# Kernel tuning notes

Measured on AMD Instinct MI355X. Metric: run time of the kernel, lower is better.

The kernel has to match this reference:

```python
import jax, jax.numpy as jnp
import numpy as np

NUM_QUERIES, NUM_KEYS = 32, 64
QUERY_DIM, KEY_DIM = 512, 512
NUM_HEADS, ATTN_DIM = 8, 64
EMBED_DIM = NUM_HEADS * ATTN_DIM  # 512
OUT_DIM = 512
TEMPERATURE = float(np.sqrt(ATTN_DIM))


def setup_inputs() -> dict:
    key = jax.random.key(0)
    ks = jax.random.split(key, 6)
    b = 1.0 / TEMPERATURE
    b_p = 1.0 / float(np.sqrt(OUT_DIM))
    q = jax.random.normal(ks[0], (NUM_QUERIES, 2048, QUERY_DIM), dtype=jnp.float32)
    k = jax.random.normal(ks[1], (NUM_KEYS, 2048, KEY_DIM), dtype=jnp.float32)
    query_weight = jax.random.uniform(ks[2], (NUM_QUERIES, QUERY_DIM, EMBED_DIM), minval=-b, maxval=b, dtype=jnp.float32)
    key_weight = jax.random.uniform(ks[3], (NUM_KEYS, KEY_DIM, EMBED_DIM), minval=-b, maxval=b, dtype=jnp.float32)
    value_weight = jax.random.uniform(ks[4], (NUM_KEYS, KEY_DIM, EMBED_DIM), minval=-b, maxval=b, dtype=jnp.float32)
    proj_weight = jax.random.uniform(ks[5], (NUM_QUERIES, EMBED_DIM, OUT_DIM), minval=-b_p, maxval=b_p, dtype=jnp.float32)
    return {"q": q, "k": k, "query_weight": query_weight, "key_weight": key_weight,
            "value_weight": value_weight, "proj_weight": proj_weight}


def reference(q, k, query_weight, key_weight, value_weight, proj_weight):
    Qn, bs, _ = q.shape
    Kn = k.shape[0]
    H, D = NUM_HEADS, ATTN_DIM
    # per-slot projections: (slots, bs, embed) -> split embed into heads
    query = jnp.einsum('ibq,iqe->ibe', q, query_weight).reshape(Qn, bs, H, D)
    key_e = jnp.einsum('jbk,jke->jbe', k, key_weight).reshape(Kn, bs, H, D)
    value = jnp.einsum('jbk,jke->jbe', k, value_weight).reshape(Kn, bs, H, D)
    # logits over key slots per (batch, head, query slot)
    logits = jnp.einsum('ibhd,jbhd->bhij', query, key_e) / TEMPERATURE
    attn = jax.nn.softmax(logits, axis=-1)  # softmax over key slots
    out = jnp.einsum('bhij,jbhd->ibhd', attn, value).reshape(Qn, bs, H * D)
    out = jnp.einsum('ibe,ieo->ibo', out, proj_weight)
    return out
```

## Files before the change

kernel.cpp:

```cpp
#include <hip/hip_runtime.h>

typedef __attribute__((ext_vector_type(8))) short bf16x8;
typedef __attribute__((ext_vector_type(4))) float f32x4;
typedef __attribute__((ext_vector_type(4))) unsigned short us4;

__device__ __forceinline__ unsigned short f2bf(float f) {
    unsigned u = __builtin_bit_cast(unsigned, f);
    u += 0x7FFFu + ((u >> 16) & 1u);
    return (unsigned short)(u >> 16);
}

__device__ __forceinline__ void gl_lds16(const void* g, void* l) {
    __builtin_amdgcn_global_load_lds(
        (const __attribute__((address_space(1))) unsigned int*)g,
        (__attribute__((address_space(3))) unsigned int*)l, 16, 0, 0);
}

#define FENCE_ asm volatile("" ::: "memory")
#define BAR_ do { FENCE_; __builtin_amdgcn_s_barrier(); FENCE_; } while (0)

__global__ __launch_bounds__(256) void cast_f32_bf16(const float* __restrict__ in,
                                                     unsigned short* __restrict__ out, int n4) {
    int i = blockIdx.x * blockDim.x + threadIdx.x;
    int stride = gridDim.x * blockDim.x;
    for (; i < n4; i += stride) {
        float4 v = ((const float4*)in)[i];
        us4 o;
        o.x = f2bf(v.x); o.y = f2bf(v.y); o.z = f2bf(v.z); o.w = f2bf(v.w);
        ((us4*)out)[i] = o;
    }
}

__global__ __launch_bounds__(256) void transpose_w(const float* __restrict__ wq,
                                                   const float* __restrict__ wk,
                                                   const float* __restrict__ wv,
                                                   const float* __restrict__ wp,
                                                   unsigned short* __restrict__ Wt) {
    int sb = blockIdx.x >> 6;
    int tile = blockIdx.x & 63;
    const float* src;
    if (sb < 32)       src = wq + (size_t)sb * 262144;
    else if (sb < 96)  src = wk + (size_t)(sb - 32) * 262144;
    else if (sb < 160) src = wv + (size_t)(sb - 96) * 262144;
    else               src = wp + (size_t)(sb - 160) * 262144;
    unsigned short* dst = Wt + (size_t)sb * 262144;
    int q0 = (tile & 7) * 64, e0 = (tile >> 3) * 64;
    __shared__ float t[64][65];
    int tx = threadIdx.x & 63, ty = threadIdx.x >> 6;
    for (int i = 0; i < 16; i++) {
        int r = ty + 4 * i;
        t[r][tx] = src[(size_t)(q0 + r) * 512 + e0 + tx];
    }
    __syncthreads();
    int tx2 = threadIdx.x & 31, ty2 = threadIdx.x >> 5;
    for (int i = 0; i < 8; i++) {
        int e = ty2 + 8 * i;
        int qq = tx2 * 2;
        unsigned a = f2bf(t[qq][e]);
        unsigned bb = f2bf(t[qq + 1][e]);
        *(unsigned*)&dst[(size_t)(e0 + e) * 512 + q0 + qq] = a | (bb << 16);
    }
}

__device__ __forceinline__ void gemm256(const unsigned short* __restrict__ Ag,
                                        const unsigned short* __restrict__ Bg,
                                        unsigned short (&lds)[2][2][16384],
                                        f32x4 (&acc)[8][4]) {
    const int tid = threadIdx.x;
    const int l = tid & 63, wid = tid >> 6;
    const int wr = (wid >> 2) * 128, wc = (wid & 3) * 64;
    const int lr = l & 15, shi = l >> 4;
    const int srcs = ((l & 7) ^ ((l >> 3) & 7)) * 8;
    const int grow = l >> 3;

    bf16x8 af[4][2], bf[4][2];

#define STG_(which, hh, t) do {                                                     \
    const unsigned short* gp = (which) ? Bg : Ag;                                   \
    _Pragma("unroll")                                                               \
    for (int q = 0; q < 2; q++) {                                                   \
        int lrow = (hh) * 128 + wid * 16 + q * 8;                                   \
        gl_lds16(gp + (size_t)(lrow + grow) * 512 + (t) * 64 + srcs,                \
                 &lds[(t) & 1][which][lrow * 64]);                                  \
    } } while (0)

#define LDA_(cur, mh) do {                                                          \
    _Pragma("unroll") for (int m = 0; m < 4; m++)                                   \
    _Pragma("unroll") for (int ks = 0; ks < 2; ks++)                                \
        af[m][ks] = *(const bf16x8*)&lds[cur][0]                                    \
            [(wr + (mh) * 64 + m * 16 + lr) * 64 + ((ks * 4 + shi) ^ (l & 7)) * 8]; \
    } while (0)

#define LDB_(cur) do {                                                             \
    _Pragma("unroll") for (int n = 0; n < 4; n++)                                   \
    _Pragma("unroll") for (int ks = 0; ks < 2; ks++)                                \
        bf[n][ks] = *(const bf16x8*)&lds[cur][1]                                    \
            [(wc + n * 16 + lr) * 64 + ((ks * 4 + shi) ^ (l & 7)) * 8];             \
    } while (0)

#define MM_(mh) do {                                                                \
    __builtin_amdgcn_s_setprio(1);                                                  \
    _Pragma("unroll") for (int m = 0; m < 4; m++)                                   \
    _Pragma("unroll") for (int n = 0; n < 4; n++)                                   \
    _Pragma("unroll") for (int ks = 0; ks < 2; ks++)                                \
        acc[(mh) * 4 + m][n] = __builtin_amdgcn_mfma_f32_16x16x32_bf16(             \
            af[m][ks], bf[n][ks], acc[(mh) * 4 + m][n], 0, 0, 0);                   \
    __builtin_amdgcn_s_setprio(0);                                                  \
    } while (0)

    STG_(0, 0, 0); STG_(0, 1, 0);
    STG_(1, 0, 0); STG_(1, 1, 0);
    STG_(1, 0, 1); STG_(1, 1, 1);
    asm volatile("s_waitcnt vmcnt(4)" ::: "memory");
    BAR_;

#pragma unroll
    for (int t = 0; t < 8; t++) {
        const int cur = t & 1;
        if (t < 7) { STG_(0, 0, t + 1); STG_(0, 1, t + 1); }
        LDA_(cur, 0); LDB_(cur);
        BAR_; MM_(0); BAR_;
        if (t < 6) { STG_(1, 0, t + 2); STG_(1, 1, t + 2); }
        LDA_(cur, 1);
        BAR_; MM_(1);
        if (t < 6)       asm volatile("s_waitcnt vmcnt(4)" ::: "memory");
        else if (t == 6) asm volatile("s_waitcnt vmcnt(0)" ::: "memory");
        if (t < 7) BAR_;
    }
#undef STG_
#undef LDA_
#undef LDB_
#undef MM_
}

__global__ __launch_bounds__(512, 1) void gemm_qkv(const unsigned short* __restrict__ qb,
                                                   const unsigned short* __restrict__ kb,
                                                   const unsigned short* __restrict__ Wt,
                                                   unsigned short* __restrict__ Qs,
                                                   unsigned short* __restrict__ Ks,
                                                   unsigned short* __restrict__ Vs) {
    __shared__ __align__(16) unsigned short lds[2][2][16384];
    int bid = blockIdx.x;
    int logical = (bid & 7) * 320 + (bid >> 3);
    int sIdx, x;
    if (logical < 512) {
        int grp = logical >> 5, w = logical & 31;
        sIdx = grp * 2 + (w & 1);
        x = w >> 1;
    } else {
        int p = (logical - 512) >> 5, w = (logical - 512) & 31;
        sIdx = 32 + p * 2 + (w & 1);
        x = w >> 1;
    }
    int tm = x >> 1, tn = x & 1;
    const unsigned short* A;
    unsigned short* Cw;
    int wslot;
    if (sIdx < 32) {
        A = qb + (size_t)sIdx * 1048576; Cw = Qs + (size_t)sIdx * 1048576; wslot = sIdx;
    } else {
        int pp = sIdx - 32, ks = pp >> 1;
        A = kb + (size_t)ks * 1048576;
        if (pp & 1) { Cw = Vs + (size_t)ks * 1048576; wslot = 96 + ks; }
        else        { Cw = Ks + (size_t)ks * 1048576; wslot = 32 + ks; }
    }
    const unsigned short* B = Wt + (size_t)wslot * 262144;
    const unsigned short* Ag = A + (size_t)(tm * 256) * 512;
    const unsigned short* Bg = B + (size_t)(tn * 256) * 512;

    f32x4 acc[8][4] = {};
    gemm256(Ag, Bg, lds, acc);

    const int l = threadIdx.x & 63, wid = threadIdx.x >> 6;
    const int wm = wid >> 2, wc = (wid & 3) * 64;
    unsigned short* Cs = &lds[0][0][0];
    for (int pass = 0; pass < 2; pass++) {
        __syncthreads();
        if (wm == pass) {
            for (int m = 0; m < 8; m++)
                for (int n = 0; n < 4; n++)
                    for (int r = 0; r < 4; r++)
                        Cs[(m * 16 + (l >> 4) * 4 + r) * 264 + wc + n * 16 + (l & 15)] = f2bf(acc[m][n][r]);
        }
        __syncthreads();
        for (int rnd = 0; rnd < 8; rnd++) {
            int idx = rnd * 512 + threadIdx.x;
            int row = idx >> 5, c8 = (idx & 31) * 8;
            bf16x8 v = *(const bf16x8*)&Cs[row * 264 + c8];
            *(bf16x8*)&Cw[(size_t)(tm * 256 + pass * 128 + row) * 512 + tn * 256 + c8] = v;
        }
    }
}

__global__ __launch_bounds__(512, 1) void gemm_proj(const unsigned short* __restrict__ Ain,
                                                    const unsigned short* __restrict__ Wt,
                                                    float* __restrict__ out) {
    __shared__ __align__(16) unsigned short lds[2][2][16384];
    int bid = blockIdx.x;
    int logical = (bid & 7) * 64 + (bid >> 3);
    int s = logical >> 4, x = logical & 15;
    int tm = x >> 1, tn = x & 1;
    const unsigned short* A = Ain + (size_t)s * 1048576;
    const unsigned short* B = Wt + (size_t)(160 + s) * 262144;
    const unsigned short* Ag = A + (size_t)(tm * 256) * 512;
    const unsigned short* Bg = B + (size_t)(tn * 256) * 512;

    f32x4 acc[8][4] = {};
    gemm256(Ag, Bg, lds, acc);

    const int l = threadIdx.x & 63, wid = threadIdx.x >> 6;
    const int wm = wid >> 2, wc = (wid & 3) * 64;
    float* Cf = (float*)&lds[0][0][0];
    for (int pass = 0; pass < 4; pass++) {
        __syncthreads();
        if (wm == (pass >> 1)) {
            int mb = (pass & 1) * 4;
            for (int mm = 0; mm < 4; mm++)
                for (int n = 0; n < 4; n++)
                    for (int r = 0; r < 4; r++)
                        Cf[(mm * 16 + (l >> 4) * 4 + r) * 260 + wc + n * 16 + (l & 15)] = acc[mb + mm][n][r];
        }
        __syncthreads();
        for (int rnd = 0; rnd < 8; rnd++) {
            int idx = rnd * 512 + threadIdx.x;
            int row = idx >> 6, c4 = (idx & 63) * 4;
            float4 v = *(const float4*)&Cf[row * 260 + c4];
            *(float4*)&out[(size_t)s * 1048576 + (size_t)(tm * 256 + pass * 64 + row) * 512 + tn * 256 + c4] = v;
        }
    }
}

__global__ __launch_bounds__(256) void attn_k(const unsigned short* __restrict__ Qs,
                                              const unsigned short* __restrict__ Ks,
                                              const unsigned short* __restrict__ Vs,
                                              unsigned short* __restrict__ Aout) {
    __shared__ __align__(16) unsigned short pl[4][32 * 72];
    __shared__ __align__(16) unsigned short vt[4][64 * 88];
    const size_t SL = 1048576;
    int w = threadIdx.x >> 6, l = threadIdx.x & 63;
    int g = blockIdx.x * 4 + w;
    int b = g >> 3, h = g & 7;
    const unsigned short* Qp = Qs + (size_t)b * 512 + h * 64;
    const unsigned short* Kp = Ks + (size_t)b * 512 + h * 64;
    const unsigned short* Vp = Vs + (size_t)b * 512 + h * 64;
    int lr = l & 15, lc = l >> 4;
    unsigned short* vtw = vt[w];

    for (int jr = 0; jr < 64; jr += 8) {
        int j = jr + (l >> 3), d0 = (l & 7) * 8;
        bf16x8 v = *(const bf16x8*)&Vp[(size_t)j * SL + d0];
        for (int e = 0; e < 8; e++) vtw[(d0 + e) * 88 + j] = (unsigned short)v[e];
    }

    bf16x8 aQ[2][2], bK[4][2];
    for (int m = 0; m < 2; m++)
        for (int kc = 0; kc < 2; kc++)
            aQ[m][kc] = *(const bf16x8*)&Qp[(size_t)(m * 16 + lr) * SL + kc * 32 + lc * 8];
    for (int n = 0; n < 4; n++)
        for (int kc = 0; kc < 2; kc++)
            bK[n][kc] = *(const bf16x8*)&Kp[(size_t)(n * 16 + lr) * SL + kc * 32 + lc * 8];

    f32x4 acc[2][4] = {};
    for (int kc = 0; kc < 2; kc++)
        for (int m = 0; m < 2; m++)
            for (int n = 0; n < 4; n++)
                acc[m][n] = __builtin_amdgcn_mfma_f32_16x16x32_bf16(aQ[m][kc], bK[n][kc], acc[m][n], 0, 0, 0);

    const float sc = 0.18033688011112042f;
    for (int m = 0; m < 2; m++) {
        for (int r = 0; r < 4; r++) {
            float v = acc[m][0][r];
            for (int n = 1; n < 4; n++) v = fmaxf(v, acc[m][n][r]);
            for (int sh = 1; sh < 16; sh <<= 1) v = fmaxf(v, __shfl_xor(v, sh));
            float ssum = 0.f;
            for (int n = 0; n < 4; n++) {
                float p = exp2f((acc[m][n][r] - v) * sc);
                acc[m][n][r] = p;
                ssum += p;
            }
            for (int sh = 1; sh < 16; sh <<= 1) ssum += __shfl_xor(ssum, sh);
            float inv = 1.0f / ssum;
            for (int n = 0; n < 4; n++)
                pl[w][(m * 16 + lc * 4 + r) * 72 + n * 16 + lr] = f2bf(acc[m][n][r] * inv);
        }
    }

    bf16x8 aP[2][2], bV[4][2];
    for (int m = 0; m < 2; m++)
        for (int kc = 0; kc < 2; kc++)
            aP[m][kc] = *(const bf16x8*)&pl[w][(m * 16 + lr) * 72 + kc * 32 + lc * 8];
    for (int n = 0; n < 4; n++)
        for (int kc = 0; kc < 2; kc++)
            bV[n][kc] = *(const bf16x8*)&vtw[(n * 16 + lr) * 88 + kc * 32 + lc * 8];

    f32x4 o[2][4] = {};
    for (int kc = 0; kc < 2; kc++)
        for (int m = 0; m < 2; m++)
            for (int n = 0; n < 4; n++)
                o[m][n] = __builtin_amdgcn_mfma_f32_16x16x32_bf16(aP[m][kc], bV[n][kc], o[m][n], 0, 0, 0);

    for (int m = 0; m < 2; m++)
        for (int n = 0; n < 4; n++)
            for (int r = 0; r < 4; r++)
                vtw[(m * 16 + lc * 4 + r) * 88 + n * 16 + lr] = f2bf(o[m][n][r]);
    for (int rnd = 0; rnd < 4; rnd++) {
        int i = rnd * 8 + (l >> 3), d0 = (l & 7) * 8;
        bf16x8 v = *(const bf16x8*)&vtw[i * 88 + d0];
        *(bf16x8*)&Aout[(size_t)i * SL + (size_t)b * 512 + h * 64 + d0] = v;
    }
}

extern "C" void kernel_launch(void* const* d_in, const int* in_sizes, int n_in,
                              void* d_out, int out_size, void* d_ws, size_t ws_size,
                              hipStream_t stream) {
    const float* q  = (const float*)d_in[0];
    const float* k  = (const float*)d_in[1];
    const float* wq = (const float*)d_in[2];
    const float* wk = (const float*)d_in[3];
    const float* wv = (const float*)d_in[4];
    const float* wp = (const float*)d_in[5];

    char* ws = (char*)d_ws;
    unsigned short* qb = (unsigned short*)(ws);
    unsigned short* kb = (unsigned short*)(ws + ((size_t)64 << 20));
    unsigned short* Wt = (unsigned short*)(ws + ((size_t)192 << 20));
    unsigned short* Qs = (unsigned short*)(ws + ((size_t)288 << 20));
    unsigned short* Ks = (unsigned short*)(ws + ((size_t)352 << 20));
    unsigned short* Vs = (unsigned short*)(ws + ((size_t)480 << 20));
    unsigned short* Aout = qb;
    float* out = (float*)d_out;

    hipLaunchKernelGGL(cast_f32_bf16, dim3(2048), dim3(256), 0, stream, q, qb, 32 * 2048 * 512 / 4);
    hipLaunchKernelGGL(cast_f32_bf16, dim3(2048), dim3(256), 0, stream, k, kb, 64 * 2048 * 512 / 4);
    hipLaunchKernelGGL(transpose_w, dim3(192 * 64), dim3(256), 0, stream, wq, wk, wv, wp, Wt);
    hipLaunchKernelGGL(gemm_qkv, dim3(2560), dim3(512), 0, stream, qb, kb, Wt, Qs, Ks, Vs);
    hipLaunchKernelGGL(attn_k, dim3(4096), dim3(256), 0, stream, Qs, Ks, Vs, Aout);
    hipLaunchKernelGGL(gemm_proj, dim3(512), dim3(512), 0, stream, Aout, Wt, out);
}
```

Before: 554.4 us.

## Fuse f32-to-bf16 input casting into QKV GEMM A-tile loading

Removes the two standalone cast kernels and instead has the QKV GEMM load fp32 activations into registers, convert them with packed bf16 conversion instructions, and write them into swizzled LDS, while B tiles still use direct global-to-LDS loads. This drops a full read/write pass over the 384 MB of q/k data plus the intermediate bf16 buffers. In exchange, A traffic doubles in bytes per GEMM tile, since each A tile is reread by the two N-tiles as fp32. The change also uses more registers for staging and needs extra VALU conversion work inside the pipelined loop.

```diff
diff --git a/kernel.cpp b/kernel.cpp
--- a/kernel.cpp
+++ b/kernel.cpp
@@ -18,18 +18,6 @@
 
 #define FENCE_ asm volatile("" ::: "memory")
 #define BAR_ do { FENCE_; __builtin_amdgcn_s_barrier(); FENCE_; } while (0)
-
-__global__ __launch_bounds__(256) void cast_f32_bf16(const float* __restrict__ in,
-                                                     unsigned short* __restrict__ out, int n4) {
-    int i = blockIdx.x * blockDim.x + threadIdx.x;
-    int stride = gridDim.x * blockDim.x;
-    for (; i < n4; i += stride) {
-        float4 v = ((const float4*)in)[i];
-        us4 o;
-        o.x = f2bf(v.x); o.y = f2bf(v.y); o.z = f2bf(v.z); o.w = f2bf(v.w);
-        ((us4*)out)[i] = o;
-    }
-}
 
 __global__ __launch_bounds__(256) void transpose_w(const float* __restrict__ wq,
                                                    const float* __restrict__ wk,
@@ -133,8 +121,111 @@
 #undef MM_
 }
 
-__global__ __launch_bounds__(512, 1) void gemm_qkv(const unsigned short* __restrict__ qb,
-                                                   const unsigned short* __restrict__ kb,
+__device__ __forceinline__ void gemm256f(const float* __restrict__ Af,
+                                         const unsigned short* __restrict__ Bg,
+                                         unsigned short (&lds)[2][2][16384],
+                                         f32x4 (&acc)[8][4]) {
+    const int tid = threadIdx.x;
+    const int l = tid & 63, wid = tid >> 6;
+    const int wr = (wid >> 2) * 128, wc = (wid & 3) * 64;
+    const int lr = l & 15, shi = l >> 4;
+    const int srcs = ((l & 7) ^ ((l >> 3) & 7)) * 8;
+    const int grow = l >> 3;
+    const int aswz = ((l & 7) ^ ((l >> 3) & 7)) * 8;
+
+    float4 rS0[8], rS1[8];
+    bf16x8 af[4][2], bf[4][2];
+
+#define LOADA_(S, t) do {                                                           \
+    _Pragma("unroll") for (int j = 0; j < 4; j++) {                                 \
+        const float* rp = Af + (size_t)(wid * 32 + j * 8 + (l >> 3)) * 512          \
+                          + (t) * 64 + (l & 7) * 8;                                 \
+        S[j * 2]     = *(const float4*)rp;                                          \
+        S[j * 2 + 1] = *(const float4*)(rp + 4);                                    \
+    } } while (0)
+
+#define WRITEA_(S, t) do {                                                          \
+    _Pragma("unroll") for (int j = 0; j < 4; j++) {                                 \
+        int row_ = wid * 32 + j * 8 + (l >> 3);                                     \
+        unsigned p0, p1, p2, p3;                                                    \
+        asm("v_cvt_pk_bf16_f32 %0, %1, %2" : "=v"(p0) : "v"(S[j*2].x),   "v"(S[j*2].y));   \
+        asm("v_cvt_pk_bf16_f32 %0, %1, %2" : "=v"(p1) : "v"(S[j*2].z),   "v"(S[j*2].w));   \
+        asm("v_cvt_pk_bf16_f32 %0, %1, %2" : "=v"(p2) : "v"(S[j*2+1].x), "v"(S[j*2+1].y)); \
+        asm("v_cvt_pk_bf16_f32 %0, %1, %2" : "=v"(p3) : "v"(S[j*2+1].z), "v"(S[j*2+1].w)); \
+        uint4 pk_; pk_.x = p0; pk_.y = p1; pk_.z = p2; pk_.w = p3;                  \
+        *(uint4*)&lds[(t) & 1][0][row_ * 64 + aswz] = pk_;                          \
+    } } while (0)
+
+#define STGB_(hh, t) do {                                                           \
+    _Pragma("unroll")                                                               \
+    for (int q = 0; q < 2; q++) {                                                   \
+        int lrow = (hh) * 128 + wid * 16 + q * 8;                                   \
+        gl_lds16(Bg + (size_t)(lrow + grow) * 512 + (t) * 64 + srcs,                \
+                 &lds[(t) & 1][1][lrow * 64]);                                      \
+    } } while (0)
+
+#define LDA_(cur, mh) do {                                                          \
+    _Pragma("unroll") for (int m = 0; m < 4; m++)                                   \
+    _Pragma("unroll") for (int ks = 0; ks < 2; ks++)                                \
+        af[m][ks] = *(const bf16x8*)&lds[cur][0]                                    \
+            [(wr + (mh) * 64 + m * 16 + lr) * 64 + ((ks * 4 + shi) ^ (l & 7)) * 8]; \
+    } while (0)
+
+#define LDB_(cur) do {                                                             \
+    _Pragma("unroll") for (int n = 0; n < 4; n++)                                   \
+    _Pragma("unroll") for (int ks = 0; ks < 2; ks++)                                \
+        bf[n][ks] = *(const bf16x8*)&lds[cur][1]                                    \
+            [(wc + n * 16 + lr) * 64 + ((ks * 4 + shi) ^ (l & 7)) * 8];             \
+    } while (0)
+
+#define MM_(mh) do {                                                                \
+    __builtin_amdgcn_s_setprio(1);                                                  \
+    _Pragma("unroll") for (int m = 0; m < 4; m++)                                   \
+    _Pragma("unroll") for (int n = 0; n < 4; n++)                                   \
+    _Pragma("unroll") for (int ks = 0; ks < 2; ks++)                                \
+        acc[(mh) * 4 + m][n] = __builtin_amdgcn_mfma_f32_16x16x32_bf16(             \
+            af[m][ks], bf[n][ks], acc[(mh) * 4 + m][n], 0, 0, 0);                   \
+    __builtin_amdgcn_s_setprio(0);                                                  \
+    } while (0)
+
+    LOADA_(rS0, 0); STGB_(0, 0); STGB_(1, 0);
+    LOADA_(rS1, 1); STGB_(0, 1); STGB_(1, 1);
+    WRITEA_(rS0, 0);
+    asm volatile("s_waitcnt lgkmcnt(0)" ::: "memory");
+    asm volatile("s_waitcnt vmcnt(12)" ::: "memory");
+    BAR_;
+
+#pragma unroll
+    for (int t = 0; t < 8; t++) {
+        const int cur = t & 1;
+        if (t < 7) {
+            if (((t + 1) & 1) == 0) WRITEA_(rS0, t + 1);
+            else                    WRITEA_(rS1, t + 1);
+        }
+        LDA_(cur, 0); LDB_(cur);
+        BAR_; MM_(0); BAR_;
+        if (t < 6) {
+            if (((t + 2) & 1) == 0) LOADA_(rS0, t + 2);
+            else                    LOADA_(rS1, t + 2);
+            STGB_(0, t + 2); STGB_(1, t + 2);
+        }
+        LDA_(cur, 1);
+        BAR_; MM_(1);
+        asm volatile("s_waitcnt lgkmcnt(0)" ::: "memory");
+        if (t < 6)       asm volatile("s_waitcnt vmcnt(12)" ::: "memory");
+        else if (t == 6) asm volatile("s_waitcnt vmcnt(0)" ::: "memory");
+        if (t < 7) BAR_;
+    }
+#undef LOADA_
+#undef WRITEA_
+#undef STGB_
+#undef LDA_
+#undef LDB_
+#undef MM_
+}
+
+__global__ __launch_bounds__(512, 1) void gemm_qkv(const float* __restrict__ qf,
+                                                   const float* __restrict__ kf,
                                                    const unsigned short* __restrict__ Wt,
                                                    unsigned short* __restrict__ Qs,
                                                    unsigned short* __restrict__ Ks,
@@ -153,23 +244,23 @@
         x = w >> 1;
     }
     int tm = x >> 1, tn = x & 1;
-    const unsigned short* A;
+    const float* Afull;
     unsigned short* Cw;
     int wslot;
     if (sIdx < 32) {
-        A = qb + (size_t)sIdx * 1048576; Cw = Qs + (size_t)sIdx * 1048576; wslot = sIdx;
+        Afull = qf + (size_t)sIdx * 1048576; Cw = Qs + (size_t)sIdx * 1048576; wslot = sIdx;
     } else {
         int pp = sIdx - 32, ks = pp >> 1;
-        A = kb + (size_t)ks * 1048576;
+        Afull = kf + (size_t)ks * 1048576;
         if (pp & 1) { Cw = Vs + (size_t)ks * 1048576; wslot = 96 + ks; }
         else        { Cw = Ks + (size_t)ks * 1048576; wslot = 32 + ks; }
     }
     const unsigned short* B = Wt + (size_t)wslot * 262144;
-    const unsigned short* Ag = A + (size_t)(tm * 256) * 512;
+    const float* Ag = Afull + (size_t)(tm * 256) * 512;
     const unsigned short* Bg = B + (size_t)(tn * 256) * 512;
 
     f32x4 acc[8][4] = {};
-    gemm256(Ag, Bg, lds, acc);
+    gemm256f(Ag, Bg, lds, acc);
 
     const int l = threadIdx.x & 63, wid = threadIdx.x >> 6;
     const int wm = wid >> 2, wc = (wid & 3) * 64;
@@ -321,19 +412,15 @@
     const float* wp = (const float*)d_in[5];
 
     char* ws = (char*)d_ws;
-    unsigned short* qb = (unsigned short*)(ws);
-    unsigned short* kb = (unsigned short*)(ws + ((size_t)64 << 20));
+    unsigned short* Aout = (unsigned short*)(ws);
     unsigned short* Wt = (unsigned short*)(ws + ((size_t)192 << 20));
     unsigned short* Qs = (unsigned short*)(ws + ((size_t)288 << 20));
     unsigned short* Ks = (unsigned short*)(ws + ((size_t)352 << 20));
     unsigned short* Vs = (unsigned short*)(ws + ((size_t)480 << 20));
-    unsigned short* Aout = qb;
     float* out = (float*)d_out;
 
-    hipLaunchKernelGGL(cast_f32_bf16, dim3(2048), dim3(256), 0, stream, q, qb, 32 * 2048 * 512 / 4);
-    hipLaunchKernelGGL(cast_f32_bf16, dim3(2048), dim3(256), 0, stream, k, kb, 64 * 2048 * 512 / 4);
     hipLaunchKernelGGL(transpose_w, dim3(192 * 64), dim3(256), 0, stream, wq, wk, wv, wp, Wt);
-    hipLaunchKernelGGL(gemm_qkv, dim3(2560), dim3(512), 0, stream, qb, kb, Wt, Qs, Ks, Vs);
+    hipLaunchKernelGGL(gemm_qkv, dim3(2560), dim3(512), 0, stream, q, k, Wt, Qs, Ks, Vs);
     hipLaunchKernelGGL(attn_k, dim3(4096), dim3(256), 0, stream, Qs, Ks, Vs, Aout);
     hipLaunchKernelGGL(gemm_proj, dim3(512), dim3(512), 0, stream, Aout, Wt, out);
 }
```

New measurement: 666.4 us. 1.2x slower.
